# Kernel tuning notes

Measured on AMD Instinct MI355X. Metric: run time of the kernel, lower is better.

## Reference

```python
import jax, jax.numpy as jnp
import numpy as np

D_MODEL = 2048
NUM_HEADS = 32
NUM_KV_HEADS = 8
D_K = D_MODEL // NUM_HEADS
B, S = 2, 2048


def setup_inputs() -> dict:
    key = jax.random.key(0)
    ks = jax.random.split(key, 6)
    sc = 1.0 / np.sqrt(D_MODEL)
    x = jax.random.normal(ks[0], (B, S, D_MODEL), dtype=jnp.float32)
    mask = jnp.tril(jnp.ones((S, S), dtype=jnp.float32))[None, None]  # [1,1,S,S]
    return {
        'x': x,
        'mask': mask,
        'Wq': jax.random.normal(ks[1], (D_MODEL, D_MODEL), jnp.float32) * sc,
        'bq': jnp.zeros((D_MODEL,), jnp.float32),
        'Wk': jax.random.normal(ks[2], (D_MODEL, NUM_KV_HEADS * D_K), jnp.float32) * sc,
        'bk': jnp.zeros((NUM_KV_HEADS * D_K,), jnp.float32),
        'Wv': jax.random.normal(ks[3], (D_MODEL, NUM_KV_HEADS * D_K), jnp.float32) * sc,
        'bv': jnp.zeros((NUM_KV_HEADS * D_K,), jnp.float32),
        'Wo': jax.random.normal(ks[4], (D_MODEL, D_MODEL), jnp.float32) * sc,
        'bo': jnp.zeros((D_MODEL,), jnp.float32),
    }


def reference(x, mask, Wq, bq, Wk, bk, Wv, bv, Wo, bo):
    b, s, _ = x.shape
    g = NUM_HEADS // NUM_KV_HEADS  # queries per kv head
    Q = (x @ Wq + bq).reshape(b, s, NUM_HEADS, D_K).transpose(0, 2, 1, 3)      # [b,h,s,dk]
    K = (x @ Wk + bk).reshape(b, s, NUM_KV_HEADS, D_K).transpose(0, 2, 1, 3)   # [b,kv,s,dk]
    V = (x @ Wv + bv).reshape(b, s, NUM_KV_HEADS, D_K).transpose(0, 2, 1, 3)
    # group queries per kv head instead of repeat_interleave on K/V
    Qg = Q.reshape(b, NUM_KV_HEADS, g, s, D_K)
    scores = jnp.einsum('bkgqd,bkld->bkgql', Qg, K) / np.sqrt(D_K)             # [b,kv,g,s,s]
    scores = jnp.where(mask[:, :, None] == 0, -1e9, scores)
    attn = jax.nn.softmax(scores, axis=-1)
    out = jnp.einsum('bkgql,bkld->bkgqd', attn, V)                              # [b,kv,g,s,dk]
    out = out.reshape(b, NUM_HEADS, s, D_K).transpose(0, 2, 1, 3).reshape(b, s, D_MODEL)
    return out @ Wo + bo
```

## Files before the change

### kernel.cpp

```cpp
#include <hip/hip_runtime.h>
#include <stdint.h>

typedef __bf16 bf16x8 __attribute__((ext_vector_type(8)));
typedef float  f32x4  __attribute__((ext_vector_type(4)));

__device__ __forceinline__ f32x4 mfma16(bf16x8 a, bf16x8 b, f32x4 c) {
    return __builtin_amdgcn_mfma_f32_16x16x32_bf16(a, b, c, 0, 0, 0);
}

__device__ __forceinline__ uint16_t f2bf(float f) {
    union { __bf16 b; uint16_t u; } cv; cv.b = (__bf16)f; return cv.u;
}

typedef __attribute__((address_space(3))) void as3_void;
typedef __attribute__((address_space(1))) void as1_void;
__device__ __forceinline__ void async_ld16(const void* g, void* l) {
    __builtin_amdgcn_global_load_lds((const as1_void*)g, (as3_void*)l, 16, 0, 0);
}


__global__ void convert_bias(const float* __restrict__ in, uint16_t* __restrict__ out,
                             const float* __restrict__ bq, const float* __restrict__ bk,
                             const float* __restrict__ bv, float* __restrict__ biasq) {
    if (blockIdx.x < 8192) {
        int i = (blockIdx.x * 256 + threadIdx.x) * 4;
        float4 v = *(const float4*)(in + i);
        ushort4 o;
        o.x = f2bf(v.x); o.y = f2bf(v.y); o.z = f2bf(v.z); o.w = f2bf(v.w);
        *(ushort4*)(out + i) = o;
    } else {
        int i = (blockIdx.x - 8192) * 256 + threadIdx.x;
        if (i < 3072)
            biasq[i] = (i < 2048) ? bq[i] : (i < 2560 ? bk[i - 2048] : bv[i - 2560]);
    }
}

__global__ void transpose_w(const float* __restrict__ Wq, const float* __restrict__ Wk,
                            const float* __restrict__ Wv, const float* __restrict__ Wo,
                            uint16_t* __restrict__ wqkvT, uint16_t* __restrict__ woT) {
    __shared__ float tile[32][33];
    const int z = blockIdx.z;
    const float* in; uint16_t* out; int ldin, off;
    if (z == 0)      { in = Wq; out = wqkvT; ldin = 2048; off = 0; }
    else if (z == 1) { if (blockIdx.x >= 16) return; in = Wk; out = wqkvT; ldin = 512; off = 2048; }
    else if (z == 2) { if (blockIdx.x >= 16) return; in = Wv; out = wqkvT; ldin = 512; off = 2560; }
    else             { in = Wo; out = woT;   ldin = 2048; off = 0; }
    const int c0 = blockIdx.x << 5, r0 = blockIdx.y << 5;
    const int tx = threadIdx.x, ty = threadIdx.y;
#pragma unroll
    for (int i = 0; i < 4; ++i)
        tile[ty + i * 8][tx] = in[(size_t)(r0 + ty + i * 8) * ldin + c0 + tx];
    __syncthreads();
#pragma unroll
    for (int i = 0; i < 4; ++i)
        out[(size_t)(off + c0 + ty + i * 8) * 2048 + r0 + tx] = f2bf(tile[tx][ty + i * 8]);
}

__global__ void transpose_v(const uint16_t* __restrict__ qkv, uint16_t* __restrict__ vt) {
    __shared__ uint16_t tile[32][33];
    const int c0 = blockIdx.x << 5, r0 = blockIdx.y << 5, b = blockIdx.z;
    const int tx = threadIdx.x, ty = threadIdx.y;
#pragma unroll
    for (int i = 0; i < 4; ++i)
        tile[ty + i * 8][tx] = qkv[(size_t)(b * 2048 + r0 + ty + i * 8) * 3072 + 2560 + c0 + tx];
    __syncthreads();
    const int perm = 4 * (tx >> 3) + (((tx & 7) < 4) ? 0 : 16) + (tx & 3);
#pragma unroll
    for (int i = 0; i < 4; ++i)
        vt[(size_t)(b * 512 + c0 + ty + i * 8) * 2048 + r0 + tx] = tile[perm][ty + i * 8];
}

template <bool F32OUT>
__global__ __launch_bounds__(256, 2)
void gemm_bt(const uint16_t* __restrict__ A, const uint16_t* __restrict__ Bt,
             const float* __restrict__ bias, void* __restrict__ Cout, int N, int K) {
    __shared__ __align__(16) uint16_t As[8192];
    __shared__ __align__(16) uint16_t Bs[8192];
    const int tid = threadIdx.x;
    const int wv = tid >> 6, ln = tid & 63;
    const int quad = ln >> 4, l16 = ln & 15;
    const int row0 = blockIdx.y << 7, col0 = blockIdx.x << 7;
    const int wm = wv >> 1, wn = wv & 1;

    const uint16_t* gA[4];
    const uint16_t* gB[4];
#pragma unroll
    for (int j = 0; j < 4; ++j) {
        int p = j * 256 + tid;
        int r = p >> 3, c = (p & 7) ^ ((r ^ (r >> 3)) & 7);
        gA[j] = A + (size_t)(row0 + r) * K + (c << 3);
        gB[j] = Bt + (size_t)(col0 + r) * K + (c << 3);
    }

    int a_off[4][2], b_off[4][2];
#pragma unroll
    for (int t = 0; t < 4; ++t)
#pragma unroll
        for (int s = 0; s < 2; ++s) {
            int r = (wm << 6) + (t << 4) + l16;
            a_off[t][s] = (((r << 3) + ((4 * s + quad) ^ ((r ^ (r >> 3)) & 7))) << 3);
            r = (wn << 6) + (t << 4) + l16;
            b_off[t][s] = (((r << 3) + ((4 * s + quad) ^ ((r ^ (r >> 3)) & 7))) << 3);
        }

    f32x4 acc[4][4] = {};

    for (int k0 = 0; k0 < K; k0 += 64) {
        __syncthreads();
#pragma unroll
        for (int j = 0; j < 4; ++j) {
            async_ld16(gA[j] + k0, As + (j << 11) + (wv << 9));
            async_ld16(gB[j] + k0, Bs + (j << 11) + (wv << 9));
        }
        __syncthreads();
#pragma unroll
        for (int s = 0; s < 2; ++s) {
            bf16x8 af[4], bfr[4];
#pragma unroll
            for (int t = 0; t < 4; ++t) af[t] = *(const bf16x8*)(As + a_off[t][s]);
#pragma unroll
            for (int t = 0; t < 4; ++t) bfr[t] = *(const bf16x8*)(Bs + b_off[t][s]);
#pragma unroll
            for (int mt = 0; mt < 4; ++mt)
#pragma unroll
                for (int nt = 0; nt < 4; ++nt)
                    acc[mt][nt] = mfma16(af[mt], bfr[nt], acc[mt][nt]);
        }
    }

#pragma unroll
    for (int nt = 0; nt < 4; ++nt) {
        const int col = col0 + (wn << 6) + (nt << 4) + l16;
        const float bv = bias[col];
#pragma unroll
        for (int mt = 0; mt < 4; ++mt) {
            const int rbase = row0 + (wm << 6) + (mt << 4) + (quad << 2);
#pragma unroll
            for (int r = 0; r < 4; ++r) {
                float v = acc[mt][nt][r] + bv;
                if (F32OUT)
                    ((float*)Cout)[(size_t)(rbase + r) * N + col] = v;
                else
                    ((uint16_t*)Cout)[(size_t)(rbase + r) * N + col] = f2bf(v);
            }
        }
    }
}

__global__ __launch_bounds__(256, 2)
void attn_fwd(const uint16_t* __restrict__ QKV, const uint16_t* __restrict__ Vt,
              uint16_t* __restrict__ AO) {
    __shared__ __align__(16) uint16_t Ks[2][4096];
    __shared__ __align__(16) uint16_t Vs[2][4096];
    __shared__ __align__(16) uint16_t Ot[4][2176];

    const int tid = threadIdx.x;
    const int wv = tid >> 6, ln = tid & 63;
    const int quad = ln >> 4, l16 = ln & 15;
    const int p = blockIdx.x, kvh = blockIdx.y, b = blockIdx.z;
    const int h = kvh * 4 + wv;

    const uint16_t* Kg = QKV + (size_t)(b * 2048) * 3072 + 2048 + kvh * 64;
    const uint16_t* Vg = Vt + (size_t)(b * 512 + kvh * 64) * 2048;

    const uint16_t* gK[2];
    const uint16_t* gV[2];
#pragma unroll
    for (int j = 0; j < 2; ++j) {
        int pos = j * 256 + tid;
        int r = pos >> 3, c = (pos & 7) ^ ((r ^ (r >> 3)) & 7);
        gK[j] = Kg + (size_t)r * 3072 + (c << 3);
        gV[j] = Vg + (size_t)r * 2048 + (c << 3);
    }
    const int sdst = wv << 9;

    int kf_off[4][2], vf_off[2][4];
#pragma unroll
    for (int g = 0; g < 4; ++g) {
        int r = g * 16 + l16, gs = (r ^ (r >> 3)) & 7;
#pragma unroll
        for (int kk = 0; kk < 2; ++kk)
            kf_off[g][kk] = ((r << 3) + ((kk * 4 + quad) ^ gs)) << 3;
    }
#pragma unroll
    for (int nt = 0; nt < 4; ++nt) {
        int r = nt * 16 + l16, gs = (r ^ (r >> 3)) & 7;
#pragma unroll
        for (int s = 0; s < 2; ++s)
            vf_off[s][nt] = ((r << 3) + ((s * 4 + quad) ^ gs)) << 3;
    }

#define EXP_PV(MASKED)                                                         \
    _Pragma("unroll")                                                          \
    for (int m = 0; m < 2; ++m) {                                              \
        float e[4][4];                                                         \
        _Pragma("unroll")                                                      \
        for (int g = 0; g < 4; ++g)                                            \
            _Pragma("unroll")                                                  \
            for (int rr = 0; rr < 4; ++rr) {                                   \
                float v = __expf(fmaf(sv[m][g][rr], 0.125f, -16.0f));          \
                if (MASKED && (16 * g + 4 * quad + rr >                        \
                               32 * wr + 16 * m + l16)) v = 0.0f;              \
                e[g][rr] = v;                                                  \
            }                                                                  \
        lp[m] += ((((e[0][0] + e[0][1]) + (e[0][2] + e[0][3]))                 \
                +  ((e[1][0] + e[1][1]) + (e[1][2] + e[1][3])))                \
                + (((e[2][0] + e[2][1]) + (e[2][2] + e[2][3]))                 \
                +  ((e[3][0] + e[3][1]) + (e[3][2] + e[3][3]))));              \
        bf16x8 pf0, pf1;                                                       \
        _Pragma("unroll")                                                      \
        for (int rr = 0; rr < 4; ++rr) {                                       \
            pf0[rr] = (__bf16)e[0][rr]; pf0[4 + rr] = (__bf16)e[1][rr];        \
            pf1[rr] = (__bf16)e[2][rr]; pf1[4 + rr] = (__bf16)e[3][rr];        \
        }                                                                      \
        _Pragma("unroll")                                                      \
        for (int nt = 0; nt < 4; ++nt) {                                       \
            acc[m][nt] = mfma16(vf[0][nt], pf0, acc[m][nt]);                   \
            acc[m][nt] = mfma16(vf[1][nt], pf1, acc[m][nt]);                   \
        }                                                                      \
    }

#pragma unroll
    for (int half = 0; half < 2; ++half) {
        const int w = half ? (63 - p) : p;
        const int q0 = w << 5;
        const int nkb = (w >> 1) + 1;
        const int wr = w & 1;

        bf16x8 qf[2][2];
#pragma unroll
        for (int m = 0; m < 2; ++m)
#pragma unroll
            for (int kk = 0; kk < 2; ++kk)
                qf[m][kk] = *(const bf16x8*)(QKV +
                    (size_t)(b * 2048 + q0 + m * 16 + l16) * 3072 + h * 64 + kk * 32 + quad * 8);

        f32x4 acc[2][4] = {};
        float lp[2] = {0.0f, 0.0f};

        __syncthreads();
#pragma unroll
        for (int j = 0; j < 2; ++j) {
            async_ld16(gK[j], Ks[0] + (j << 11) + sdst);
            async_ld16(gV[j], Vs[0] + (j << 11) + sdst);
        }

        for (int t = 0; t < nkb; ++t) {
            const int cur = t & 1;
            __syncthreads();
            if (t + 1 < nkb) {
                const size_t ko = (size_t)((t + 1) << 6) * 3072;
                const int vo = (t + 1) << 6;
#pragma unroll
                for (int j = 0; j < 2; ++j) {
                    async_ld16(gK[j] + ko, Ks[cur ^ 1] + (j << 11) + sdst);
                    async_ld16(gV[j] + vo, Vs[cur ^ 1] + (j << 11) + sdst);
                }
            }

            bf16x8 kf[4][2], vf[2][4];
#pragma unroll
            for (int g = 0; g < 4; ++g)
#pragma unroll
                for (int kk = 0; kk < 2; ++kk)
                    kf[g][kk] = *(const bf16x8*)(Ks[cur] + kf_off[g][kk]);
#pragma unroll
            for (int s = 0; s < 2; ++s)
#pragma unroll
                for (int nt = 0; nt < 4; ++nt)
                    vf[s][nt] = *(const bf16x8*)(Vs[cur] + vf_off[s][nt]);

            f32x4 sv[2][4];
#pragma unroll
            for (int m = 0; m < 2; ++m)
#pragma unroll
                for (int g = 0; g < 4; ++g) {
                    f32x4 z = {0.f, 0.f, 0.f, 0.f};
                    z = mfma16(kf[g][0], qf[m][0], z);
                    z = mfma16(kf[g][1], qf[m][1], z);
                    sv[m][g] = z;
                }

            if (t < nkb - 1) {
                EXP_PV(false)
            } else {
                EXP_PV(true)
            }
        }

        float inv[2];
#pragma unroll
        for (int m = 0; m < 2; ++m) {
            float rs = lp[m];
            rs += __shfl_xor(rs, 16, 64);
            rs += __shfl_xor(rs, 32, 64);
            inv[m] = 1.0f / rs;
        }

        uint16_t* ot = Ot[wv];
#pragma unroll
        for (int m = 0; m < 2; ++m)
#pragma unroll
            for (int nt = 0; nt < 4; ++nt)
#pragma unroll
                for (int pp = 0; pp < 2; ++pp) {
                    uint32_t pk = (uint32_t)f2bf(acc[m][nt][2 * pp] * inv[m]) |
                                  ((uint32_t)f2bf(acc[m][nt][2 * pp + 1] * inv[m]) << 16);
                    *(uint32_t*)(ot + (m * 16 + l16) * 68 + nt * 16 + quad * 4 + 2 * pp) = pk;
                }
        const int orow = ln >> 1, ohalf = (ln & 1) << 5;
        uint16_t* aobase = AO + (size_t)(b * 2048 + q0 + orow) * 2048 + h * 64 + ohalf;
        const uint16_t* osrc = ot + orow * 68 + ohalf;
#pragma unroll
        for (int c4 = 0; c4 < 4; ++c4)
            *(uint4*)(aobase + c4 * 8) = *(const uint4*)(osrc + c4 * 8);
    }
#undef EXP_PV
}


extern "C" void kernel_launch(void* const* d_in, const int* in_sizes, int n_in,
                              void* d_out, int out_size, void* d_ws, size_t ws_size,
                              hipStream_t stream) {
    (void)in_sizes; (void)n_in; (void)out_size; (void)ws_size;
    const float* x  = (const float*)d_in[0];
    const float* Wq = (const float*)d_in[2];
    const float* bq = (const float*)d_in[3];
    const float* Wk = (const float*)d_in[4];
    const float* bk = (const float*)d_in[5];
    const float* Wv = (const float*)d_in[6];
    const float* bv = (const float*)d_in[7];
    const float* Wo = (const float*)d_in[8];
    const float* bo = (const float*)d_in[9];

    char* ws = (char*)d_ws;
    uint16_t* xb    = (uint16_t*)ws;
    uint16_t* wqkvT = (uint16_t*)(ws + 16777216);
    uint16_t* woT   = (uint16_t*)(ws + 16777216 + 12582912);
    float*    biasq = (float*)(ws + 16777216 + 12582912 + 8388608);
    uint16_t* qkv   = (uint16_t*)d_out;
    uint16_t* ao    = xb;
    uint16_t* vt    = wqkvT;

    dim3 tb(32, 8);
    convert_bias<<<8204, 256, 0, stream>>>(x, xb, bq, bk, bv, biasq);
    transpose_w<<<dim3(64, 64, 4), tb, 0, stream>>>(Wq, Wk, Wv, Wo, wqkvT, woT);
    gemm_bt<false><<<dim3(24, 32), 256, 0, stream>>>(xb, wqkvT, biasq, qkv, 3072, 2048);
    transpose_v<<<dim3(16, 64, 2), tb, 0, stream>>>(qkv, vt);
    attn_fwd<<<dim3(32, 8, 2), 256, 0, stream>>>(qkv, vt, ao);
    gemm_bt<true><<<dim3(16, 32), 256, 0, stream>>>(ao, woT, bo, d_out, 2048, 2048);
}
```

Measured before the change: 290.9 us.

## Use exp2 with folded constants, perm-based bf16 packing, and MFMA row sums

Replaces __expf with a native exp2 whose scale and offset are pre-multiplied by log2e. bf16 packing now uses a byte perm that truncates instead of rounding. The softmax denominator is computed by an extra MFMA against a ones vector on the packed bf16 probabilities, removing the scalar add tree and cross-lane shuffles. This trades VALU work for two more MFMAs per step, and it changes numerics: the row sums now come from the truncated bf16 values, and the probabilities are truncated rather than rounded.

```diff
diff --git a/kernel.cpp b/kernel.cpp
--- a/kernel.cpp
+++ b/kernel.cpp
@@ -3,6 +3,7 @@
 
 typedef __bf16 bf16x8 __attribute__((ext_vector_type(8)));
 typedef float  f32x4  __attribute__((ext_vector_type(4)));
+typedef uint32_t u32x4 __attribute__((ext_vector_type(4)));
 
 __device__ __forceinline__ f32x4 mfma16(bf16x8 a, bf16x8 b, f32x4 c) {
     return __builtin_amdgcn_mfma_f32_16x16x32_bf16(a, b, c, 0, 0, 0);
@@ -11,6 +12,20 @@
 __device__ __forceinline__ uint16_t f2bf(float f) {
     union { __bf16 b; uint16_t u; } cv; cv.b = (__bf16)f; return cv.u;
 }
+
+__device__ __forceinline__ uint32_t pkbf(float lo, float hi) {
+    union { float f; uint32_t u; } a, b;
+    a.f = hi; b.f = lo;
+    return __builtin_amdgcn_perm(a.u, b.u, 0x07060302u);
+}
+
+#if __has_builtin(__builtin_amdgcn_exp2f)
+#define EXP2F(x) __builtin_amdgcn_exp2f(x)
+#else
+#define EXP2F(x) exp2f(x)
+#endif
+#define EXP_C1 0.18033688f
+#define EXP_C2 -23.0831206f
 
 typedef __attribute__((address_space(3))) void as3_void;
 typedef __attribute__((address_space(1))) void as1_void;
@@ -190,6 +205,10 @@
             vf_off[s][nt] = ((r << 3) + ((s * 4 + quad) ^ gs)) << 3;
     }
 
+    bf16x8 ones;
+#pragma unroll
+    for (int j = 0; j < 8; ++j) ones[j] = (__bf16)1.0f;
+
 #define EXP_PV(MASKED)                                                         \
     _Pragma("unroll")                                                          \
     for (int m = 0; m < 2; ++m) {                                              \
@@ -198,21 +217,23 @@
         for (int g = 0; g < 4; ++g)                                            \
             _Pragma("unroll")                                                  \
             for (int rr = 0; rr < 4; ++rr) {                                   \
-                float v = __expf(fmaf(sv[m][g][rr], 0.125f, -16.0f));          \
+                float v = EXP2F(fmaf(sv[m][g][rr], EXP_C1, EXP_C2));           \
                 if (MASKED && (16 * g + 4 * quad + rr >                        \
                                32 * wr + 16 * m + l16)) v = 0.0f;              \
                 e[g][rr] = v;                                                  \
             }                                                                  \
-        lp[m] += ((((e[0][0] + e[0][1]) + (e[0][2] + e[0][3]))                 \
-                +  ((e[1][0] + e[1][1]) + (e[1][2] + e[1][3])))                \
-                + (((e[2][0] + e[2][1]) + (e[2][2] + e[2][3]))                 \
-                +  ((e[3][0] + e[3][1]) + (e[3][2] + e[3][3]))));              \
-        bf16x8 pf0, pf1;                                                       \
+        u32x4 p0, p1;                                                          \
         _Pragma("unroll")                                                      \
-        for (int rr = 0; rr < 4; ++rr) {                                       \
-            pf0[rr] = (__bf16)e[0][rr]; pf0[4 + rr] = (__bf16)e[1][rr];        \
-            pf1[rr] = (__bf16)e[2][rr]; pf1[4 + rr] = (__bf16)e[3][rr];        \
+        for (int d = 0; d < 2; ++d) {                                          \
+            p0[d]     = pkbf(e[0][2 * d], e[0][2 * d + 1]);                    \
+            p0[2 + d] = pkbf(e[1][2 * d], e[1][2 * d + 1]);                    \
+            p1[d]     = pkbf(e[2][2 * d], e[2][2 * d + 1]);                    \
+            p1[2 + d] = pkbf(e[3][2 * d], e[3][2 * d + 1]);                    \
         }                                                                      \
+        bf16x8 pf0 = __builtin_bit_cast(bf16x8, p0);                           \
+        bf16x8 pf1 = __builtin_bit_cast(bf16x8, p1);                           \
+        lacc[m] = mfma16(ones, pf0, lacc[m]);                                  \
+        lacc[m] = mfma16(ones, pf1, lacc[m]);                                  \
         _Pragma("unroll")                                                      \
         for (int nt = 0; nt < 4; ++nt) {                                       \
             acc[m][nt] = mfma16(vf[0][nt], pf0, acc[m][nt]);                   \
@@ -236,7 +257,7 @@
                     (size_t)(b * 2048 + q0 + m * 16 + l16) * 3072 + h * 64 + kk * 32 + quad * 8);
 
         f32x4 acc[2][4] = {};
-        float lp[2] = {0.0f, 0.0f};
+        f32x4 lacc[2] = {};
 
         __syncthreads();
 #pragma unroll
@@ -290,12 +311,7 @@
 
         float inv[2];
 #pragma unroll
-        for (int m = 0; m < 2; ++m) {
-            float rs = lp[m];
-            rs += __shfl_xor(rs, 16, 64);
-            rs += __shfl_xor(rs, 32, 64);
-            inv[m] = 1.0f / rs;
-        }
+        for (int m = 0; m < 2; ++m) inv[m] = 1.0f / lacc[m][0];
 
         uint16_t* ot = Ot[wv];
 #pragma unroll
```

Result: slower. 298.1 us (+2.5%).
